# Kernel optimization log

Measured on AMD Instinct MI355X. Metric: run time of the kernel, lower is better.

Reference implementation:

```python
import jax, jax.numpy as jnp
import numpy as np

N, E, C, H, L = 20000, 200000, 64, 4, 2
L0_IN, E_IN, L0_OUT = 65, 15, 64
HC = H * C
EPS = 1e-5  # InstanceNorm1d default eps
NEG_SLOPE = 0.01  # F.leaky_relu default used by DGL EGATConv


def setup_inputs() -> dict:
    key = jax.random.key(0)
    ks = jax.random.split(key, 16)
    def s(k, shape, fan):
        return (jax.random.normal(k, shape, jnp.float32) / np.float32(np.sqrt(fan)))
    return {
        "x": jax.random.normal(ks[0], (N, L0_IN), jnp.float32),
        "efeat": jax.random.normal(ks[1], (E, E_IN), jnp.float32),
        "src": jax.random.randint(ks[2], (E,), 0, N, dtype=jnp.int32),
        "dst": jax.random.randint(ks[3], (E,), 0, N, dtype=jnp.int32),
        "Wn0": s(ks[4], (L0_IN, C), L0_IN),
        "bn0": jnp.zeros((C,), jnp.float32),
        "We0": s(ks[5], (E_IN, C), E_IN),
        "be0": jnp.zeros((C,), jnp.float32),
        "Wnode": s(ks[6], (L, C, HC), C),
        "bnode": jnp.zeros((L, HC), jnp.float32),
        "Wni": s(ks[7], (L, C, HC), C),
        "Wnj": s(ks[8], (L, C, HC), C),
        "Wfij": s(ks[9], (L, C, HC), C),
        "attn": s(ks[10], (L, H, C), C),
        "bias_e": jnp.zeros((L, HC), jnp.float32),
        "Wf": s(ks[11], (C, L0_OUT), C),
        "bf": jnp.zeros((L0_OUT,), jnp.float32),
    }


def _inorm(x):
    # InstanceNorm1d on a 2D [rows, channels] tensor == per-row normalization
    m = jnp.mean(x, axis=-1, keepdims=True)
    v = jnp.var(x, axis=-1, keepdims=True)
    return (x - m) * jax.lax.rsqrt(v + EPS)


def reference(x, efeat, src, dst, Wn0, bn0, We0, be0, Wnode, bnode,
              Wni, Wnj, Wfij, attn, bias_e, Wf, bf):
    h = x @ Wn0 + bn0        # [N, C]
    f = efeat @ We0 + be0    # [E, C]
    for l in range(L):
        # edge feature update: f_out = fc_ni(h)[src] + fc_nj(h)[dst] + fc_fij(f) + bias
        f_out = (h @ Wni[l])[src] + (h @ Wnj[l])[dst] + f @ Wfij[l] + bias_e[l]  # [E, HC]
        e = jax.nn.leaky_relu(f_out, NEG_SLOPE).reshape(E, H, C)
        score = jnp.einsum('ehc,hc->eh', e, attn[l])  # [E, H]
        # edge softmax over incoming edges of each destination node
        smax = jax.ops.segment_max(score, dst, num_segments=N)
        w = jnp.exp(score - smax[dst])
        denom = jax.ops.segment_sum(w, dst, num_segments=N)
        a = w / denom[dst]                                # [E, H]
        hproj = (h @ Wnode[l] + bnode[l]).reshape(N, H, C)
        msg = hproj[src] * a[:, :, None]                  # [E, H, C]
        h_new = jax.ops.segment_sum(msg, dst, num_segments=N)  # [N, H, C]
        # mean over heads -> InstanceNorm -> ELU
        h = jax.nn.elu(_inorm(jnp.mean(h_new, axis=1)))
        f = jax.nn.elu(_inorm(jnp.mean(f_out.reshape(E, H, C), axis=1)))
    return h @ Wf + bf
```

## Files before the change

kernel.cpp:

```cpp
#include <hip/hip_runtime.h>
#include <cmath>

#define NN 20000
#define NE 200000
#define SCAN_BLOCKS 79
#define EBLK 3125
#define EBLK_P 391

typedef __attribute__((ext_vector_type(8))) short bf16x8;
typedef __attribute__((ext_vector_type(4))) float f32x4;
typedef unsigned int uint;

__device__ __forceinline__ float4 ld4(const float* p){ return *(const float4*)p; }

__device__ __forceinline__ uint packbf(float a, float b) {
  uint ua = __float_as_uint(a);
  uint ub = __float_as_uint(b);
  ua = (ua + 0x7fffu + ((ua >> 16) & 1u)) >> 16;
  ub = (ub + 0x7fffu + ((ub >> 16) & 1u)) >> 16;
  return ua | (ub << 16);
}
__device__ __forceinline__ float4 up4(uint2 u) {
  return make_float4(__uint_as_float(u.x << 16), __uint_as_float(u.x & 0xffff0000u),
                     __uint_as_float(u.y << 16), __uint_as_float(u.y & 0xffff0000u));
}

__global__ void gemm16_bf16(const float* __restrict__ A, const float* __restrict__ B,
                            const float* __restrict__ bias, uint2* __restrict__ O,
                            int M, int K, const int* __restrict__ map) {
  int idx = blockIdx.x * 256 + threadIdx.x;
  if (idx >= M * 4) return;
  int m = idx >> 2, jq = idx & 3;
  const float* a = A + (long)m * K;
  const float* b = B + jq * 16;
  float c00=0,c01=0,c02=0,c03=0,c04=0,c05=0,c06=0,c07=0;
  float c08=0,c09=0,c10=0,c11=0,c12=0,c13=0,c14=0,c15=0;
  for (int k = 0; k < K; k++) {
    float av = a[k];
    const float* br = b + (long)k * 64;
    float4 b0 = ld4(br), b1 = ld4(br + 4), b2 = ld4(br + 8), b3 = ld4(br + 12);
    c00 = fmaf(av, b0.x, c00); c01 = fmaf(av, b0.y, c01); c02 = fmaf(av, b0.z, c02); c03 = fmaf(av, b0.w, c03);
    c04 = fmaf(av, b1.x, c04); c05 = fmaf(av, b1.y, c05); c06 = fmaf(av, b1.z, c06); c07 = fmaf(av, b1.w, c07);
    c08 = fmaf(av, b2.x, c08); c09 = fmaf(av, b2.y, c09); c10 = fmaf(av, b2.z, c10); c11 = fmaf(av, b2.w, c11);
    c12 = fmaf(av, b3.x, c12); c13 = fmaf(av, b3.y, c13); c14 = fmaf(av, b3.z, c14); c15 = fmaf(av, b3.w, c15);
  }
  const float* bb = bias + jq * 16;
  float4 v0 = ld4(bb), v1 = ld4(bb + 4), v2 = ld4(bb + 8), v3 = ld4(bb + 12);
  int mo = map ? map[m] : m;
  uint2* op = O + (long)mo * 16 + jq * 4;
  op[0] = make_uint2(packbf(c00 + v0.x, c01 + v0.y), packbf(c02 + v0.z, c03 + v0.w));
  op[1] = make_uint2(packbf(c04 + v1.x, c05 + v1.y), packbf(c06 + v1.z, c07 + v1.w));
  op[2] = make_uint2(packbf(c08 + v2.x, c09 + v2.y), packbf(c10 + v2.z, c11 + v2.w));
  op[3] = make_uint2(packbf(c12 + v3.x, c13 + v3.y), packbf(c14 + v3.z, c15 + v3.w));
}

__global__ void zero_i32(int* __restrict__ p, int n) {
  int i = blockIdx.x * 256 + threadIdx.x;
  if (i < n) p[i] = 0;
}

__global__ void count_deg(const int* __restrict__ dst, int* __restrict__ deg) {
  int e = blockIdx.x * 256 + threadIdx.x;
  if (e < NE) atomicAdd(&deg[dst[e]], 1);
}

__global__ void scan1(const int* __restrict__ deg, int* __restrict__ off, int* __restrict__ bsum) {
  __shared__ int buf[256];
  int t = threadIdx.x;
  int g = blockIdx.x * 256 + t;
  int v = (g < NN) ? deg[g] : 0;
  buf[t] = v;
  __syncthreads();
  for (int s = 1; s < 256; s <<= 1) {
    int x = (t >= s) ? buf[t - s] : 0;
    __syncthreads();
    buf[t] += x;
    __syncthreads();
  }
  if (g < NN) off[g] = buf[t] - v;
  if (t == 255) bsum[blockIdx.x] = buf[255];
}

__global__ void scan2(int* __restrict__ bsum, int* __restrict__ off) {
  __shared__ int buf[128];
  int t = threadIdx.x;
  int v = (t < SCAN_BLOCKS) ? bsum[t] : 0;
  buf[t] = v;
  __syncthreads();
  for (int s = 1; s < 128; s <<= 1) {
    int x = (t >= s) ? buf[t - s] : 0;
    __syncthreads();
    buf[t] += x;
    __syncthreads();
  }
  if (t < SCAN_BLOCKS) bsum[t] = buf[t] - v;
  if (t == 127) off[NN] = buf[127];
}

__global__ void scan3(int* __restrict__ off, const int* __restrict__ bsum) {
  int g = blockIdx.x * 256 + threadIdx.x;
  if (g < NN) off[g] += bsum[blockIdx.x];
}

__global__ void fill_csr(const int* __restrict__ dst, const int* __restrict__ src,
                         const int* __restrict__ off, int* __restrict__ cursor,
                         int* __restrict__ esrc, int* __restrict__ edst,
                         int* __restrict__ csr_pos) {
  int e = blockIdx.x * 256 + threadIdx.x;
  if (e >= NE) return;
  int d = dst[e];
  int p = atomicAdd(&cursor[d], 1);
  int pos = off[d] + p;
  esrc[pos] = src[e];
  edst[pos] = d;
  csr_pos[e] = pos;
}

__global__ void prep_w(const float* __restrict__ Wni, const float* __restrict__ Wnj,
                       const float* __restrict__ Wfij, const float* __restrict__ Wnode,
                       const float* __restrict__ bnode,
                       uint* __restrict__ Wcat, uint* __restrict__ WcT,
                       float* __restrict__ bmean) {
  int rid = blockIdx.x * 256 + threadIdx.x;
  if (rid < 512) {
    int l = rid >> 8, c = rid & 255;
    uint* D = Wcat + (size_t)l * 24576 + c * 96;
    for (int k8 = 0; k8 < 24; k8++) {
      int ss = k8 >> 3;
      const float* S = (ss == 0 ? Wni : ss == 1 ? Wnj : Wfij) + l * 16384;
      int kl = (k8 & 7) * 8;
      uint u0 = packbf(S[(kl+0)*256 + c], S[(kl+1)*256 + c]);
      uint u1 = packbf(S[(kl+2)*256 + c], S[(kl+3)*256 + c]);
      uint u2 = packbf(S[(kl+4)*256 + c], S[(kl+5)*256 + c]);
      uint u3 = packbf(S[(kl+6)*256 + c], S[(kl+7)*256 + c]);
      *((uint4*)(D + k8 * 4)) = make_uint4(u0, u1, u2, u3);
    }
  } else if (rid < 640) {
    int idx = rid - 512;
    int l = idx >> 6, c = idx & 63;
    const float* S = Wnode + l * 16384;
    uint* D = WcT + (size_t)l * 8192 + c * 128;
    for (int kp = 0; kp < 128; kp++) {
      int k0 = kp * 2, k1 = kp * 2 + 1;
      float v0 = S[(k0 & 63) * 256 + (k0 >> 6) * 64 + c] * 0.25f;
      float v1 = S[(k1 & 63) * 256 + (k1 >> 6) * 64 + c] * 0.25f;
      D[kp] = packbf(v0, v1);
    }
  } else if (rid < 768) {
    int idx = rid - 640;
    int l = idx >> 6, c = idx & 63;
    const float* S = bnode + l * 256;
    bmean[l * 64 + c] = 0.25f * (S[c] + S[64 + c] + S[128 + c] + S[192 + c]);
  }
}

__global__ __launch_bounds__(256) void edge_mfma(
    const uint4* __restrict__ f_bf, const uint4* __restrict__ h_bf,
    const uint* __restrict__ Wcat_l, const float* __restrict__ be_l,
    const float* __restrict__ attn_l, const int* __restrict__ esrc,
    const int* __restrict__ edst, float* __restrict__ scc,
    uint4* __restrict__ f_next4)
{
  int nb = (blockIdx.x & 7) * EBLK_P + (blockIdx.x >> 3);
  if (nb >= EBLK) return;
  int base = nb * 64;
  __shared__ uint bstage[2][96 * 36];
  __shared__ float red[4][2][33][6];
  int t = threadIdx.x, lane = t & 63, w = t >> 6;
  int col = lane & 15, quad = lane >> 4;
  int sr = t >> 3, sc = t & 7;
  {
    int e0 = base + sr;
    uint4 vs = h_bf[(long)esrc[e0] * 8 + sc];
    uint4 vd = h_bf[(long)edst[e0] * 8 + sc];
    uint4 vf = f_bf[(long)e0 * 8 + sc];
    *(uint4*)&bstage[0][sr * 36 + sc * 4] = vs;
    *(uint4*)&bstage[0][(32 + sr) * 36 + sc * 4] = vd;
    *(uint4*)&bstage[0][(64 + sr) * 36 + sc * 4] = vf;
  }
  int e1 = base + 32 + sr;
  uint4 v1s = h_bf[(long)esrc[e1] * 8 + sc];
  uint4 v1d = h_bf[(long)edst[e1] * 8 + sc];
  uint4 v1f = f_bf[(long)e1 * 8 + sc];
  __syncthreads();
  float ma[2][2][4];
  #pragma unroll
  for (int ch = 0; ch < 2; ch++) {
    const uint* bp = &bstage[ch][0];
    bf16x8 Ba[6], Bb[6];
    Ba[0] = *(const bf16x8*)&bp[col * 36 + quad * 4];
    Ba[1] = *(const bf16x8*)&bp[col * 36 + 16 + quad * 4];
    Ba[2] = *(const bf16x8*)&bp[(32 + col) * 36 + quad * 4];
    Ba[3] = *(const bf16x8*)&bp[(32 + col) * 36 + 16 + quad * 4];
    Ba[4] = *(const bf16x8*)&bp[(64 + col) * 36 + quad * 4];
    Ba[5] = *(const bf16x8*)&bp[(64 + col) * 36 + 16 + quad * 4];
    Bb[0] = *(const bf16x8*)&bp[(16 + col) * 36 + quad * 4];
    Bb[1] = *(const bf16x8*)&bp[(16 + col) * 36 + 16 + quad * 4];
    Bb[2] = *(const bf16x8*)&bp[(48 + col) * 36 + quad * 4];
    Bb[3] = *(const bf16x8*)&bp[(48 + col) * 36 + 16 + quad * 4];
    Bb[4] = *(const bf16x8*)&bp[(80 + col) * 36 + quad * 4];
    Bb[5] = *(const bf16x8*)&bp[(80 + col) * 36 + 16 + quad * 4];
    float ma0 = 0.f, ma1 = 0.f, ma2 = 0.f, ma3 = 0.f;
    float mb0 = 0.f, mb1 = 0.f, mb2 = 0.f, mb3 = 0.f;
    float sa0 = 0.f, sa1 = 0.f, sa2 = 0.f, sa3 = 0.f;
    float sb0 = 0.f, sb1 = 0.f, sb2 = 0.f, sb3 = 0.f;
    #pragma unroll
    for (int hg = 0; hg < 4; hg++) {
      f32x4 aa = (f32x4){0.f, 0.f, 0.f, 0.f};
      f32x4 ab = (f32x4){0.f, 0.f, 0.f, 0.f};
      const uint* Ab = &Wcat_l[((4 * hg + w) * 16 + col) * 96 + quad * 4];
      #pragma unroll
      for (int kt = 0; kt < 6; kt++) {
        bf16x8 Af = *(const bf16x8*)(Ab + kt * 16);
        aa = __builtin_amdgcn_mfma_f32_16x16x32_bf16(Af, Ba[kt], aa, 0, 0, 0);
        ab = __builtin_amdgcn_mfma_f32_16x16x32_bf16(Af, Bb[kt], ab, 0, 0, 0);
      }
      int ce = (4 * hg + w) * 16 + quad * 4;
      float4 be4 = ld4(be_l + ce);
      float4 at4 = ld4(attn_l + ce);
      float xa0 = aa[0] + be4.x, xa1 = aa[1] + be4.y;
      float xa2 = aa[2] + be4.z, xa3 = aa[3] + be4.w;
      float xb0 = ab[0] + be4.x, xb1 = ab[1] + be4.y;
      float xb2 = ab[2] + be4.z, xb3 = ab[3] + be4.w;
      float la0 = xa0 > 0.f ? xa0 : 0.01f * xa0;
      float la1 = xa1 > 0.f ? xa1 : 0.01f * xa1;
      float la2 = xa2 > 0.f ? xa2 : 0.01f * xa2;
      float la3 = xa3 > 0.f ? xa3 : 0.01f * xa3;
      float lb0 = xb0 > 0.f ? xb0 : 0.01f * xb0;
      float lb1 = xb1 > 0.f ? xb1 : 0.01f * xb1;
      float lb2 = xb2 > 0.f ? xb2 : 0.01f * xb2;
      float lb3 = xb3 > 0.f ? xb3 : 0.01f * xb3;
      float dpa = la0 * at4.x + la1 * at4.y + la2 * at4.z + la3 * at4.w;
      float dpb = lb0 * at4.x + lb1 * at4.y + lb2 * at4.z + lb3 * at4.w;
      if (hg == 0) { sa0 = dpa; sb0 = dpb; }
      else if (hg == 1) { sa1 = dpa; sb1 = dpb; }
      else if (hg == 2) { sa2 = dpa; sb2 = dpb; }
      else { sa3 = dpa; sb3 = dpb; }
      ma0 += xa0; ma1 += xa1; ma2 += xa2; ma3 += xa3;
      mb0 += xb0; mb1 += xb1; mb2 += xb2; mb3 += xb3;
    }
    ma0 *= 0.25f; ma1 *= 0.25f; ma2 *= 0.25f; ma3 *= 0.25f;
    mb0 *= 0.25f; mb1 *= 0.25f; mb2 *= 0.25f; mb3 *= 0.25f;
    ma[ch][0][0] = ma0; ma[ch][0][1] = ma1; ma[ch][0][2] = ma2; ma[ch][0][3] = ma3;
    ma[ch][1][0] = mb0; ma[ch][1][1] = mb1; ma[ch][1][2] = mb2; ma[ch][1][3] = mb3;
    float s1a = ma0 + ma1 + ma2 + ma3;
    float s2a = ma0*ma0 + ma1*ma1 + ma2*ma2 + ma3*ma3;
    float s1b = mb0 + mb1 + mb2 + mb3;
    float s2b = mb0*mb0 + mb1*mb1 + mb2*mb2 + mb3*mb3;
    sa0 += __shfl_xor(sa0, 16); sa0 += __shfl_xor(sa0, 32);
    sa1 += __shfl_xor(sa1, 16); sa1 += __shfl_xor(sa1, 32);
    sa2 += __shfl_xor(sa2, 16); sa2 += __shfl_xor(sa2, 32);
    sa3 += __shfl_xor(sa3, 16); sa3 += __shfl_xor(sa3, 32);
    sb0 += __shfl_xor(sb0, 16); sb0 += __shfl_xor(sb0, 32);
    sb1 += __shfl_xor(sb1, 16); sb1 += __shfl_xor(sb1, 32);
    sb2 += __shfl_xor(sb2, 16); sb2 += __shfl_xor(sb2, 32);
    sb3 += __shfl_xor(sb3, 16); sb3 += __shfl_xor(sb3, 32);
    s1a += __shfl_xor(s1a, 16); s1a += __shfl_xor(s1a, 32);
    s2a += __shfl_xor(s2a, 16); s2a += __shfl_xor(s2a, 32);
    s1b += __shfl_xor(s1b, 16); s1b += __shfl_xor(s1b, 32);
    s2b += __shfl_xor(s2b, 16); s2b += __shfl_xor(s2b, 32);
    if (quad == 0) {
      float* ra = &red[w][ch][col][0];
      ra[0] = sa0; ra[1] = sa1; ra[2] = sa2; ra[3] = sa3; ra[4] = s1a; ra[5] = s2a;
      float* rb = &red[w][ch][16 + col][0];
      rb[0] = sb0; rb[1] = sb1; rb[2] = sb2; rb[3] = sb3; rb[4] = s1b; rb[5] = s2b;
    }
    if (ch == 0) {
      *(uint4*)&bstage[1][sr * 36 + sc * 4] = v1s;
      *(uint4*)&bstage[1][(32 + sr) * 36 + sc * 4] = v1d;
      *(uint4*)&bstage[1][(64 + sr) * 36 + sc * 4] = v1f;
      __syncthreads();
    }
  }
  __syncthreads();
  {
    int eL = t >> 2, hh = t & 3;
    int chx = eL >> 5, c32 = eL & 31;
    float sv = red[0][chx][c32][hh] + red[1][chx][c32][hh]
             + red[2][chx][c32][hh] + red[3][chx][c32][hh];
    scc[(long)(base + eL) * 4 + hh] = sv;
  }
  uint* fout = &bstage[0][0];
  #pragma unroll
  for (int ch = 0; ch < 2; ch++) {
    #pragma unroll
    for (int sub = 0; sub < 2; sub++) {
      int c32 = sub * 16 + col;
      float s1T = red[0][ch][c32][4] + red[1][ch][c32][4]
                + red[2][ch][c32][4] + red[3][ch][c32][4];
      float s2T = red[0][ch][c32][5] + red[1][ch][c32][5]
                + red[2][ch][c32][5] + red[3][ch][c32][5];
      float mean = s1T * 0.015625f;
      float var  = s2T * 0.015625f - mean * mean;
      float rs = rsqrtf(var + 1e-5f);
      float o0 = (ma[ch][sub][0] - mean) * rs; o0 = o0 > 0.f ? o0 : expm1f(o0);
      float o1 = (ma[ch][sub][1] - mean) * rs; o1 = o1 > 0.f ? o1 : expm1f(o1);
      float o2 = (ma[ch][sub][2] - mean) * rs; o2 = o2 > 0.f ? o2 : expm1f(o2);
      float o3 = (ma[ch][sub][3] - mean) * rs; o3 = o3 > 0.f ? o3 : expm1f(o3);
      int eL = ch * 32 + c32;
      fout[eL * 36 + w * 8 + quad * 2]     = packbf(o0, o1);
      fout[eL * 36 + w * 8 + quad * 2 + 1] = packbf(o2, o3);
    }
  }
  __syncthreads();
  {
    int row = t >> 2, part = t & 3;
    uint4 x0 = *(uint4*)&fout[row * 36 + part * 8];
    uint4 x1 = *(uint4*)&fout[row * 36 + part * 8 + 4];
    long gp = ((long)(base + row)) * 8 + part * 2;
    f_next4[gp] = x0;
    f_next4[gp + 1] = x1;
  }
}

__global__ __launch_bounds__(256) void agg_combine(
    const uint2* __restrict__ h2, const float4* __restrict__ sc_csr4,
    const int* __restrict__ esrc, const int* __restrict__ off,
    const uint4* __restrict__ WcT4, const float* __restrict__ bmean_l,
    uint4* __restrict__ h_next4)
{
  __shared__ uint gsh[16][132];
  __shared__ float red2[4][17][2];
  __shared__ uint fout2[16 * 36];
  int t = threadIdx.x, lane = t & 63, w = t >> 6;
  int col = lane & 15, quad = lane >> 4;
  int n0 = blockIdx.x * 16;
  bf16x8 A2[8];
  #pragma unroll
  for (int kt = 0; kt < 8; kt++)
    A2[kt] = *(const bf16x8*)&WcT4[(w * 16 + col) * 32 + kt * 4 + quad];
  #pragma unroll 1
  for (int nl = 0; nl < 4; nl++) {
    int n = n0 + w * 4 + nl;
    int o0 = off[n], o1 = off[n + 1];
    float mx0 = -3.0e38f, mx1 = -3.0e38f, mx2 = -3.0e38f, mx3 = -3.0e38f;
    for (int i = o0 + quad; i < o1; i += 4) {
      float4 s = sc_csr4[i];
      mx0 = fmaxf(mx0, s.x); mx1 = fmaxf(mx1, s.y);
      mx2 = fmaxf(mx2, s.z); mx3 = fmaxf(mx3, s.w);
    }
    mx0 = fmaxf(mx0, __shfl_xor(mx0, 16)); mx0 = fmaxf(mx0, __shfl_xor(mx0, 32));
    mx1 = fmaxf(mx1, __shfl_xor(mx1, 16)); mx1 = fmaxf(mx1, __shfl_xor(mx1, 32));
    mx2 = fmaxf(mx2, __shfl_xor(mx2, 16)); mx2 = fmaxf(mx2, __shfl_xor(mx2, 32));
    mx3 = fmaxf(mx3, __shfl_xor(mx3, 16)); mx3 = fmaxf(mx3, __shfl_xor(mx3, 32));
    float d0 = 0.f, d1 = 0.f, d2 = 0.f, d3 = 0.f;
    float a00=0.f,a01=0.f,a02=0.f,a03=0.f, a10=0.f,a11=0.f,a12=0.f,a13=0.f;
    float a20=0.f,a21=0.f,a22=0.f,a23=0.f, a30=0.f,a31=0.f,a32=0.f,a33=0.f;
    for (int i = o0 + quad; i < o1; i += 4) {
      float4 s = sc_csr4[i];
      float w0 = __expf(s.x - mx0), w1 = __expf(s.y - mx1);
      float w2 = __expf(s.z - mx2), w3 = __expf(s.w - mx3);
      d0 += w0; d1 += w1; d2 += w2; d3 += w3;
      uint2 hv = h2[(long)esrc[i] * 16 + col];
      float4 p = up4(hv);
      a00 = fmaf(w0,p.x,a00); a01 = fmaf(w0,p.y,a01); a02 = fmaf(w0,p.z,a02); a03 = fmaf(w0,p.w,a03);
      a10 = fmaf(w1,p.x,a10); a11 = fmaf(w1,p.y,a11); a12 = fmaf(w1,p.z,a12); a13 = fmaf(w1,p.w,a13);
      a20 = fmaf(w2,p.x,a20); a21 = fmaf(w2,p.y,a21); a22 = fmaf(w2,p.z,a22); a23 = fmaf(w2,p.w,a23);
      a30 = fmaf(w3,p.x,a30); a31 = fmaf(w3,p.y,a31); a32 = fmaf(w3,p.z,a32); a33 = fmaf(w3,p.w,a33);
    }
    d0 += __shfl_xor(d0,16); d0 += __shfl_xor(d0,32);
    d1 += __shfl_xor(d1,16); d1 += __shfl_xor(d1,32);
    d2 += __shfl_xor(d2,16); d2 += __shfl_xor(d2,32);
    d3 += __shfl_xor(d3,16); d3 += __shfl_xor(d3,32);
    a00 += __shfl_xor(a00,16); a00 += __shfl_xor(a00,32);
    a01 += __shfl_xor(a01,16); a01 += __shfl_xor(a01,32);
    a02 += __shfl_xor(a02,16); a02 += __shfl_xor(a02,32);
    a03 += __shfl_xor(a03,16); a03 += __shfl_xor(a03,32);
    a10 += __shfl_xor(a10,16); a10 += __shfl_xor(a10,32);
    a11 += __shfl_xor(a11,16); a11 += __shfl_xor(a11,32);
    a12 += __shfl_xor(a12,16); a12 += __shfl_xor(a12,32);
    a13 += __shfl_xor(a13,16); a13 += __shfl_xor(a13,32);
    a20 += __shfl_xor(a20,16); a20 += __shfl_xor(a20,32);
    a21 += __shfl_xor(a21,16); a21 += __shfl_xor(a21,32);
    a22 += __shfl_xor(a22,16); a22 += __shfl_xor(a22,32);
    a23 += __shfl_xor(a23,16); a23 += __shfl_xor(a23,32);
    a30 += __shfl_xor(a30,16); a30 += __shfl_xor(a30,32);
    a31 += __shfl_xor(a31,16); a31 += __shfl_xor(a31,32);
    a32 += __shfl_xor(a32,16); a32 += __shfl_xor(a32,32);
    a33 += __shfl_xor(a33,16); a33 += __shfl_xor(a33,32);
    uint u0 = 0u, u1 = 0u, u2 = 0u, u3 = 0u, u4 = 0u, u5 = 0u, u6 = 0u, u7 = 0u;
    if (o0 < o1) {
      float i0 = 1.f / d0, i1 = 1.f / d1, i2 = 1.f / d2, i3 = 1.f / d3;
      u0 = packbf(a00*i0, a01*i0); u1 = packbf(a02*i0, a03*i0);
      u2 = packbf(a10*i1, a11*i1); u3 = packbf(a12*i1, a13*i1);
      u4 = packbf(a20*i2, a21*i2); u5 = packbf(a22*i2, a23*i2);
      u6 = packbf(a30*i3, a31*i3); u7 = packbf(a32*i3, a33*i3);
    }
    if (quad == 0) {
      int nloc = w * 4 + nl;
      gsh[nloc][col*2]      = u0; gsh[nloc][col*2 + 1]      = u1;
      gsh[nloc][32 + col*2] = u2; gsh[nloc][32 + col*2 + 1] = u3;
      gsh[nloc][64 + col*2] = u4; gsh[nloc][64 + col*2 + 1] = u5;
      gsh[nloc][96 + col*2] = u6; gsh[nloc][96 + col*2 + 1] = u7;
    }
  }
  __syncthreads();
  f32x4 acc = (f32x4){0.f, 0.f, 0.f, 0.f};
  #pragma unroll
  for (int kt = 0; kt < 8; kt++) {
    bf16x8 Bg = *(const bf16x8*)&gsh[col][kt * 16 + quad * 4];
    acc = __builtin_amdgcn_mfma_f32_16x16x32_bf16(A2[kt], Bg, acc, 0, 0, 0);
  }
  int n2 = n0 + col;
  int dg = off[n2 + 1] - off[n2];
  float4 bm = ld4(bmean_l + w * 16 + quad * 4);
  float x0, x1, x2, x3;
  if (dg > 0) { x0 = acc[0] + bm.x; x1 = acc[1] + bm.y; x2 = acc[2] + bm.z; x3 = acc[3] + bm.w; }
  else { x0 = x1 = x2 = x3 = 0.f; }
  float s1 = x0 + x1 + x2 + x3;
  float s2 = x0*x0 + x1*x1 + x2*x2 + x3*x3;
  s1 += __shfl_xor(s1, 16); s2 += __shfl_xor(s2, 16);
  s1 += __shfl_xor(s1, 32); s2 += __shfl_xor(s2, 32);
  if (quad == 0) { red2[w][col][0] = s1; red2[w][col][1] = s2; }
  __syncthreads();
  float s1T = red2[0][col][0] + red2[1][col][0] + red2[2][col][0] + red2[3][col][0];
  float s2T = red2[0][col][1] + red2[1][col][1] + red2[2][col][1] + red2[3][col][1];
  float mean = s1T * 0.015625f;
  float var  = s2T * 0.015625f - mean * mean;
  float rs = rsqrtf(var + 1e-5f);
  float o0 = (x0 - mean) * rs; o0 = o0 > 0.f ? o0 : expm1f(o0);
  float o1 = (x1 - mean) * rs; o1 = o1 > 0.f ? o1 : expm1f(o1);
  float o2 = (x2 - mean) * rs; o2 = o2 > 0.f ? o2 : expm1f(o2);
  float o3 = (x3 - mean) * rs; o3 = o3 > 0.f ? o3 : expm1f(o3);
  fout2[col * 36 + w * 8 + quad * 2]     = packbf(o0, o1);
  fout2[col * 36 + w * 8 + quad * 2 + 1] = packbf(o2, o3);
  __syncthreads();
  if (t < 128) {
    int row = t >> 3, part = t & 7;
    uint4 x = *(uint4*)&fout2[row * 36 + part * 4];
    h_next4[((long)(n0 + row)) * 8 + part] = x;
  }
}

__global__ void final_gemm(const uint2* __restrict__ h, const float* __restrict__ Wf,
                           const float* __restrict__ bf_, float* __restrict__ out) {
  int idx = blockIdx.x * 256 + threadIdx.x;
  if (idx >= NN * 16) return;
  int m = idx >> 4, j4 = (idx & 15) << 2;
  const uint2* row = h + (long)m * 16;
  float ax = 0.f, ay = 0.f, az = 0.f, aw = 0.f;
  for (int kk = 0; kk < 16; kk++) {
    float4 a = up4(row[kk]);
    float4 b0 = ld4(Wf + (kk * 4 + 0) * 64 + j4);
    float4 b1 = ld4(Wf + (kk * 4 + 1) * 64 + j4);
    float4 b2 = ld4(Wf + (kk * 4 + 2) * 64 + j4);
    float4 b3 = ld4(Wf + (kk * 4 + 3) * 64 + j4);
    ax = fmaf(a.x, b0.x, ax); ay = fmaf(a.x, b0.y, ay); az = fmaf(a.x, b0.z, az); aw = fmaf(a.x, b0.w, aw);
    ax = fmaf(a.y, b1.x, ax); ay = fmaf(a.y, b1.y, ay); az = fmaf(a.y, b1.z, az); aw = fmaf(a.y, b1.w, aw);
    ax = fmaf(a.z, b2.x, ax); ay = fmaf(a.z, b2.y, ay); az = fmaf(a.z, b2.z, az); aw = fmaf(a.z, b2.w, aw);
    ax = fmaf(a.w, b3.x, ax); ay = fmaf(a.w, b3.y, ay); az = fmaf(a.w, b3.z, az); aw = fmaf(a.w, b3.w, aw);
  }
  float4 bb = ld4(bf_ + j4);
  *(float4*)(out + (long)m * 64 + j4) = make_float4(ax + bb.x, ay + bb.y, az + bb.z, aw + bb.w);
}

extern "C" void kernel_launch(void* const* d_in, const int* in_sizes, int n_in,
                              void* d_out, int out_size, void* d_ws, size_t ws_size,
                              hipStream_t stream) {
  const float* x      = (const float*)d_in[0];
  const float* efeat  = (const float*)d_in[1];
  const int*   src    = (const int*)d_in[2];
  const int*   dst    = (const int*)d_in[3];
  const float* Wn0    = (const float*)d_in[4];
  const float* bn0    = (const float*)d_in[5];
  const float* We0    = (const float*)d_in[6];
  const float* be0    = (const float*)d_in[7];
  const float* Wnode  = (const float*)d_in[8];
  const float* bnode  = (const float*)d_in[9];
  const float* Wni    = (const float*)d_in[10];
  const float* Wnj    = (const float*)d_in[11];
  const float* Wfij   = (const float*)d_in[12];
  const float* attn   = (const float*)d_in[13];
  const float* bias_e = (const float*)d_in[14];
  const float* Wf     = (const float*)d_in[15];
  const float* bf     = (const float*)d_in[16];
  float* out = (float*)d_out;

  char* w = (char*)d_ws;
  auto alloc = [&](size_t nbytes) { char* p = w; w += (nbytes + 255) & ~(size_t)255; return p; };
  uint2* h_a   = (uint2*)alloc((size_t)NN * 128);
  uint2* h_b   = (uint2*)alloc((size_t)NN * 128);
  uint2* f_a   = (uint2*)alloc((size_t)NE * 128);
  uint2* f_b   = (uint2*)alloc((size_t)NE * 128);
  float* scc   = (float*)alloc((size_t)NE * 16);
  uint*  Wcat  = (uint*)alloc((size_t)2 * 24576 * 4);
  uint*  WcT   = (uint*)alloc((size_t)2 * 8192 * 4);
  float* bmean = (float*)alloc((size_t)2 * 64 * 4);
  int* deg     = (int*)alloc((size_t)NN * 2 * 4);
  int* cursor  = deg + NN;
  int* off     = (int*)alloc((size_t)(NN + 1) * 4);
  int* esrc    = (int*)alloc((size_t)NE * 4);
  int* edst    = (int*)alloc((size_t)NE * 4);
  int* csr_pos = (int*)alloc((size_t)NE * 4);
  int* bsum    = (int*)alloc((size_t)128 * 4);

  zero_i32<<<(2 * NN + 255) / 256, 256, 0, stream>>>(deg, 2 * NN);
  count_deg<<<(NE + 255) / 256, 256, 0, stream>>>(dst, deg);
  scan1<<<SCAN_BLOCKS, 256, 0, stream>>>(deg, off, bsum);
  scan2<<<1, 128, 0, stream>>>(bsum, off);
  scan3<<<SCAN_BLOCKS, 256, 0, stream>>>(off, bsum);
  fill_csr<<<(NE + 255) / 256, 256, 0, stream>>>(dst, src, off, cursor, esrc, edst, csr_pos);

  gemm16_bf16<<<(NN * 4 + 255) / 256, 256, 0, stream>>>(x, Wn0, bn0, h_a, NN, 65, nullptr);
  gemm16_bf16<<<(NE * 4 + 255) / 256, 256, 0, stream>>>(efeat, We0, be0, f_a, NE, 15, csr_pos);
  prep_w<<<4, 256, 0, stream>>>(Wni, Wnj, Wfij, Wnode, bnode, Wcat, WcT, bmean);

  uint2* hc = h_a; uint2* hn = h_b;
  uint2* fc = f_a; uint2* fn = f_b;
  for (int l = 0; l < 2; l++) {
    const uint* Wcat_l = Wcat + (size_t)l * 24576;
    const uint4* WcT_l = (const uint4*)(WcT + (size_t)l * 8192);
    const float* bm_l  = bmean + (size_t)l * 64;
    const float* be_l  = bias_e + (size_t)l * 256;
    const float* at_l  = attn + (size_t)l * 256;
    edge_mfma<<<8 * EBLK_P, 256, 0, stream>>>((const uint4*)fc, (const uint4*)hc,
                                              Wcat_l, be_l, at_l, esrc, edst, scc,
                                              (uint4*)fn);
    agg_combine<<<NN / 16, 256, 0, stream>>>((const uint2*)hc, (const float4*)scc,
                                             esrc, off, WcT_l, bm_l, (uint4*)hn);
    uint2* tmp = hc; hc = hn; hn = tmp;
    tmp = fc; fc = fn; fn = tmp;
  }
  final_gemm<<<(NN * 16 + 255) / 256, 256, 0, stream>>>(hc, Wf, bf, out);
}
```

Before: 499.5 us.

## Make edge kernel persistent with cross-block prefetch and unroll aggregation loops

Turns edge_mfma into a persistent grid-stride kernel with 768 blocks. Each block prefetches the gathered rows for the next 64-edge block while it computes the current one, so gather latency overlaps with MFMA work and the XCD-aware block remapping is no longer needed. The aggregation loops in agg_combine are unrolled two-wide to expose more memory-level parallelism. The input GEMM's K is made a template parameter and the small GEMM loops get unroll pragmas. The persistent form adds a dedicated fout buffer and an extra barrier per iteration, and it uses fewer blocks than before, which may reduce occupancy.

```diff
diff --git a/kernel.cpp b/kernel.cpp
--- a/kernel.cpp
+++ b/kernel.cpp
@@ -5,7 +5,7 @@
 #define NE 200000
 #define SCAN_BLOCKS 79
 #define EBLK 3125
-#define EBLK_P 391
+#define GRID_E 768
 
 typedef __attribute__((ext_vector_type(8))) short bf16x8;
 typedef __attribute__((ext_vector_type(4))) float f32x4;
@@ -25,9 +25,10 @@
                      __uint_as_float(u.y << 16), __uint_as_float(u.y & 0xffff0000u));
 }
 
+template<int K>
 __global__ void gemm16_bf16(const float* __restrict__ A, const float* __restrict__ B,
                             const float* __restrict__ bias, uint2* __restrict__ O,
-                            int M, int K, const int* __restrict__ map) {
+                            int M, const int* __restrict__ map) {
   int idx = blockIdx.x * 256 + threadIdx.x;
   if (idx >= M * 4) return;
   int m = idx >> 2, jq = idx & 3;
@@ -35,6 +36,7 @@
   const float* b = B + jq * 16;
   float c00=0,c01=0,c02=0,c03=0,c04=0,c05=0,c06=0,c07=0;
   float c08=0,c09=0,c10=0,c11=0,c12=0,c13=0,c14=0,c15=0;
+  #pragma unroll
   for (int k = 0; k < K; k++) {
     float av = a[k];
     const float* br = b + (long)k * 64;
@@ -154,6 +156,92 @@
   }
 }
 
+__device__ __forceinline__ void edge_compute(
+    const uint* bp, const uint* __restrict__ Wcat_l,
+    const float* __restrict__ be_l, const float* __restrict__ attn_l,
+    int w, int col, int quad, int ch,
+    float (&ma)[2][2][4], float (&red)[4][2][33][6])
+{
+  bf16x8 Ba[6], Bb[6];
+  Ba[0] = *(const bf16x8*)&bp[col * 36 + quad * 4];
+  Ba[1] = *(const bf16x8*)&bp[col * 36 + 16 + quad * 4];
+  Ba[2] = *(const bf16x8*)&bp[(32 + col) * 36 + quad * 4];
+  Ba[3] = *(const bf16x8*)&bp[(32 + col) * 36 + 16 + quad * 4];
+  Ba[4] = *(const bf16x8*)&bp[(64 + col) * 36 + quad * 4];
+  Ba[5] = *(const bf16x8*)&bp[(64 + col) * 36 + 16 + quad * 4];
+  Bb[0] = *(const bf16x8*)&bp[(16 + col) * 36 + quad * 4];
+  Bb[1] = *(const bf16x8*)&bp[(16 + col) * 36 + 16 + quad * 4];
+  Bb[2] = *(const bf16x8*)&bp[(48 + col) * 36 + quad * 4];
+  Bb[3] = *(const bf16x8*)&bp[(48 + col) * 36 + 16 + quad * 4];
+  Bb[4] = *(const bf16x8*)&bp[(80 + col) * 36 + quad * 4];
+  Bb[5] = *(const bf16x8*)&bp[(80 + col) * 36 + 16 + quad * 4];
+  float ma0 = 0.f, ma1 = 0.f, ma2 = 0.f, ma3 = 0.f;
+  float mb0 = 0.f, mb1 = 0.f, mb2 = 0.f, mb3 = 0.f;
+  float sa0 = 0.f, sa1 = 0.f, sa2 = 0.f, sa3 = 0.f;
+  float sb0 = 0.f, sb1 = 0.f, sb2 = 0.f, sb3 = 0.f;
+  #pragma unroll
+  for (int hg = 0; hg < 4; hg++) {
+    f32x4 aa = (f32x4){0.f, 0.f, 0.f, 0.f};
+    f32x4 ab = (f32x4){0.f, 0.f, 0.f, 0.f};
+    const uint* Ab = &Wcat_l[((4 * hg + w) * 16 + col) * 96 + quad * 4];
+    #pragma unroll
+    for (int kt = 0; kt < 6; kt++) {
+      bf16x8 Af = *(const bf16x8*)(Ab + kt * 16);
+      aa = __builtin_amdgcn_mfma_f32_16x16x32_bf16(Af, Ba[kt], aa, 0, 0, 0);
+      ab = __builtin_amdgcn_mfma_f32_16x16x32_bf16(Af, Bb[kt], ab, 0, 0, 0);
+    }
+    int ce = (4 * hg + w) * 16 + quad * 4;
+    float4 be4 = ld4(be_l + ce);
+    float4 at4 = ld4(attn_l + ce);
+    float xa0 = aa[0] + be4.x, xa1 = aa[1] + be4.y;
+    float xa2 = aa[2] + be4.z, xa3 = aa[3] + be4.w;
+    float xb0 = ab[0] + be4.x, xb1 = ab[1] + be4.y;
+    float xb2 = ab[2] + be4.z, xb3 = ab[3] + be4.w;
+    float la0 = xa0 > 0.f ? xa0 : 0.01f * xa0;
+    float la1 = xa1 > 0.f ? xa1 : 0.01f * xa1;
+    float la2 = xa2 > 0.f ? xa2 : 0.01f * xa2;
+    float la3 = xa3 > 0.f ? xa3 : 0.01f * xa3;
+    float lb0 = xb0 > 0.f ? xb0 : 0.01f * xb0;
+    float lb1 = xb1 > 0.f ? xb1 : 0.01f * xb1;
+    float lb2 = xb2 > 0.f ? xb2 : 0.01f * xb2;
+    float lb3 = xb3 > 0.f ? xb3 : 0.01f * xb3;
+    float dpa = la0 * at4.x + la1 * at4.y + la2 * at4.z + la3 * at4.w;
+    float dpb = lb0 * at4.x + lb1 * at4.y + lb2 * at4.z + lb3 * at4.w;
+    if (hg == 0) { sa0 = dpa; sb0 = dpb; }
+    else if (hg == 1) { sa1 = dpa; sb1 = dpb; }
+    else if (hg == 2) { sa2 = dpa; sb2 = dpb; }
+    else { sa3 = dpa; sb3 = dpb; }
+    ma0 += xa0; ma1 += xa1; ma2 += xa2; ma3 += xa3;
+    mb0 += xb0; mb1 += xb1; mb2 += xb2; mb3 += xb3;
+  }
+  ma0 *= 0.25f; ma1 *= 0.25f; ma2 *= 0.25f; ma3 *= 0.25f;
+  mb0 *= 0.25f; mb1 *= 0.25f; mb2 *= 0.25f; mb3 *= 0.25f;
+  ma[ch][0][0] = ma0; ma[ch][0][1] = ma1; ma[ch][0][2] = ma2; ma[ch][0][3] = ma3;
+  ma[ch][1][0] = mb0; ma[ch][1][1] = mb1; ma[ch][1][2] = mb2; ma[ch][1][3] = mb3;
+  float s1a = ma0 + ma1 + ma2 + ma3;
+  float s2a = ma0*ma0 + ma1*ma1 + ma2*ma2 + ma3*ma3;
+  float s1b = mb0 + mb1 + mb2 + mb3;
+  float s2b = mb0*mb0 + mb1*mb1 + mb2*mb2 + mb3*mb3;
+  sa0 += __shfl_xor(sa0, 16); sa0 += __shfl_xor(sa0, 32);
+  sa1 += __shfl_xor(sa1, 16); sa1 += __shfl_xor(sa1, 32);
+  sa2 += __shfl_xor(sa2, 16); sa2 += __shfl_xor(sa2, 32);
+  sa3 += __shfl_xor(sa3, 16); sa3 += __shfl_xor(sa3, 32);
+  sb0 += __shfl_xor(sb0, 16); sb0 += __shfl_xor(sb0, 32);
+  sb1 += __shfl_xor(sb1, 16); sb1 += __shfl_xor(sb1, 32);
+  sb2 += __shfl_xor(sb2, 16); sb2 += __shfl_xor(sb2, 32);
+  sb3 += __shfl_xor(sb3, 16); sb3 += __shfl_xor(sb3, 32);
+  s1a += __shfl_xor(s1a, 16); s1a += __shfl_xor(s1a, 32);
+  s2a += __shfl_xor(s2a, 16); s2a += __shfl_xor(s2a, 32);
+  s1b += __shfl_xor(s1b, 16); s1b += __shfl_xor(s1b, 32);
+  s2b += __shfl_xor(s2b, 16); s2b += __shfl_xor(s2b, 32);
+  if (quad == 0) {
+    float* ra = &red[w][ch][col][0];
+    ra[0] = sa0; ra[1] = sa1; ra[2] = sa2; ra[3] = sa3; ra[4] = s1a; ra[5] = s2a;
+    float* rb = &red[w][ch][16 + col][0];
+    rb[0] = sb0; rb[1] = sb1; rb[2] = sb2; rb[3] = sb3; rb[4] = s1b; rb[5] = s2b;
+  }
+}
+
 __global__ __launch_bounds__(256) void edge_mfma(
     const uint4* __restrict__ f_bf, const uint4* __restrict__ h_bf,
     const uint* __restrict__ Wcat_l, const float* __restrict__ be_l,
@@ -161,16 +249,14 @@
     const int* __restrict__ edst, float* __restrict__ scc,
     uint4* __restrict__ f_next4)
 {
-  int nb = (blockIdx.x & 7) * EBLK_P + (blockIdx.x >> 3);
-  if (nb >= EBLK) return;
-  int base = nb * 64;
   __shared__ uint bstage[2][96 * 36];
+  __shared__ uint fout[64 * 36];
   __shared__ float red[4][2][33][6];
   int t = threadIdx.x, lane = t & 63, w = t >> 6;
   int col = lane & 15, quad = lane >> 4;
   int sr = t >> 3, sc = t & 7;
   {
-    int e0 = base + sr;
+    int e0 = blockIdx.x * 64 + sr;
     uint4 vs = h_bf[(long)esrc[e0] * 8 + sc];
     uint4 vd = h_bf[(long)edst[e0] * 8 + sc];
     uint4 vf = f_bf[(long)e0 * 8 + sc];
@@ -178,138 +264,66 @@
     *(uint4*)&bstage[0][(32 + sr) * 36 + sc * 4] = vd;
     *(uint4*)&bstage[0][(64 + sr) * 36 + sc * 4] = vf;
   }
-  int e1 = base + 32 + sr;
-  uint4 v1s = h_bf[(long)esrc[e1] * 8 + sc];
-  uint4 v1d = h_bf[(long)edst[e1] * 8 + sc];
-  uint4 v1f = f_bf[(long)e1 * 8 + sc];
   __syncthreads();
-  float ma[2][2][4];
-  #pragma unroll
-  for (int ch = 0; ch < 2; ch++) {
-    const uint* bp = &bstage[ch][0];
-    bf16x8 Ba[6], Bb[6];
-    Ba[0] = *(const bf16x8*)&bp[col * 36 + quad * 4];
-    Ba[1] = *(const bf16x8*)&bp[col * 36 + 16 + quad * 4];
-    Ba[2] = *(const bf16x8*)&bp[(32 + col) * 36 + quad * 4];
-    Ba[3] = *(const bf16x8*)&bp[(32 + col) * 36 + 16 + quad * 4];
-    Ba[4] = *(const bf16x8*)&bp[(64 + col) * 36 + quad * 4];
-    Ba[5] = *(const bf16x8*)&bp[(64 + col) * 36 + 16 + quad * 4];
-    Bb[0] = *(const bf16x8*)&bp[(16 + col) * 36 + quad * 4];
-    Bb[1] = *(const bf16x8*)&bp[(16 + col) * 36 + 16 + quad * 4];
-    Bb[2] = *(const bf16x8*)&bp[(48 + col) * 36 + quad * 4];
-    Bb[3] = *(const bf16x8*)&bp[(48 + col) * 36 + 16 + quad * 4];
-    Bb[4] = *(const bf16x8*)&bp[(80 + col) * 36 + quad * 4];
-    Bb[5] = *(const bf16x8*)&bp[(80 + col) * 36 + 16 + quad * 4];
-    float ma0 = 0.f, ma1 = 0.f, ma2 = 0.f, ma3 = 0.f;
-    float mb0 = 0.f, mb1 = 0.f, mb2 = 0.f, mb3 = 0.f;
-    float sa0 = 0.f, sa1 = 0.f, sa2 = 0.f, sa3 = 0.f;
-    float sb0 = 0.f, sb1 = 0.f, sb2 = 0.f, sb3 = 0.f;
+  for (int nb = blockIdx.x; nb < EBLK; nb += GRID_E) {
+    int base = nb * 64;
+    int nbn = nb + GRID_E;
+    float ma[2][2][4];
+    int e1 = base + 32 + sr;
+    uint4 p1s = h_bf[(long)esrc[e1] * 8 + sc];
+    uint4 p1d = h_bf[(long)edst[e1] * 8 + sc];
+    uint4 p1f = f_bf[(long)e1 * 8 + sc];
+    edge_compute(&bstage[0][0], Wcat_l, be_l, attn_l, w, col, quad, 0, ma, red);
+    *(uint4*)&bstage[1][sr * 36 + sc * 4] = p1s;
+    *(uint4*)&bstage[1][(32 + sr) * 36 + sc * 4] = p1d;
+    *(uint4*)&bstage[1][(64 + sr) * 36 + sc * 4] = p1f;
+    int e2 = (nbn < EBLK ? nbn : nb) * 64 + sr;
+    uint4 p0s = h_bf[(long)esrc[e2] * 8 + sc];
+    uint4 p0d = h_bf[(long)edst[e2] * 8 + sc];
+    uint4 p0f = f_bf[(long)e2 * 8 + sc];
+    __syncthreads();
+    edge_compute(&bstage[1][0], Wcat_l, be_l, attn_l, w, col, quad, 1, ma, red);
+    __syncthreads();
+    {
+      int eL = t >> 2, hh = t & 3;
+      int chx = eL >> 5, c32 = eL & 31;
+      float sv = red[0][chx][c32][hh] + red[1][chx][c32][hh]
+               + red[2][chx][c32][hh] + red[3][chx][c32][hh];
+      scc[(long)(base + eL) * 4 + hh] = sv;
+    }
     #pragma unroll
-    for (int hg = 0; hg < 4; hg++) {
-      f32x4 aa = (f32x4){0.f, 0.f, 0.f, 0.f};
-      f32x4 ab = (f32x4){0.f, 0.f, 0.f, 0.f};
-      const uint* Ab = &Wcat_l[((4 * hg + w) * 16 + col) * 96 + quad * 4];
+    for (int ch = 0; ch < 2; ch++) {
       #pragma unroll
-      for (int kt = 0; kt < 6; kt++) {
-        bf16x8 Af = *(const bf16x8*)(Ab + kt * 16);
-        aa = __builtin_amdgcn_mfma_f32_16x16x32_bf16(Af, Ba[kt], aa, 0, 0, 0);
-        ab = __builtin_amdgcn_mfma_f32_16x16x32_bf16(Af, Bb[kt], ab, 0, 0, 0);
+      for (int sub = 0; sub < 2; sub++) {
+        int c32 = sub * 16 + col;
+        float s1T = red[0][ch][c32][4] + red[1][ch][c32][4]
+                  + red[2][ch][c32][4] + red[3][ch][c32][4];
+        float s2T = red[0][ch][c32][5] + red[1][ch][c32][5]
+                  + red[2][ch][c32][5] + red[3][ch][c32][5];
+        float mean = s1T * 0.015625f;
+        float var  = s2T * 0.015625f - mean * mean;
+        float rs = rsqrtf(var + 1e-5f);
+        float o0 = (ma[ch][sub][0] - mean) * rs; o0 = o0 > 0.f ? o0 : expm1f(o0);
+        float o1 = (ma[ch][sub][1] - mean) * rs; o1 = o1 > 0.f ? o1 : expm1f(o1);
+        float o2 = (ma[ch][sub][2] - mean) * rs; o2 = o2 > 0.f ? o2 : expm1f(o2);
+        float o3 = (ma[ch][sub][3] - mean) * rs; o3 = o3 > 0.f ? o3 : expm1f(o3);
+        int eL = ch * 32 + c32;
+        fout[eL * 36 + w * 8 + quad * 2]     = packbf(o0, o1);
+        fout[eL * 36 + w * 8 + quad * 2 + 1] = packbf(o2, o3);
       }
-      int ce = (4 * hg + w) * 16 + quad * 4;
-      float4 be4 = ld4(be_l + ce);
-      float4 at4 = ld4(attn_l + ce);
-      float xa0 = aa[0] + be4.x, xa1 = aa[1] + be4.y;
-      float xa2 = aa[2] + be4.z, xa3 = aa[3] + be4.w;
-      float xb0 = ab[0] + be4.x, xb1 = ab[1] + be4.y;
-      float xb2 = ab[2] + be4.z, xb3 = ab[3] + be4.w;
-      float la0 = xa0 > 0.f ? xa0 : 0.01f * xa0;
-      float la1 = xa1 > 0.f ? xa1 : 0.01f * xa1;
-      float la2 = xa2 > 0.f ? xa2 : 0.01f * xa2;
-      float la3 = xa3 > 0.f ? xa3 : 0.01f * xa3;
-      float lb0 = xb0 > 0.f ? xb0 : 0.01f * xb0;
-      float lb1 = xb1 > 0.f ? xb1 : 0.01f * xb1;
-      float lb2 = xb2 > 0.f ? xb2 : 0.01f * xb2;
-      float lb3 = xb3 > 0.f ? xb3 : 0.01f * xb3;
-      float dpa = la0 * at4.x + la1 * at4.y + la2 * at4.z + la3 * at4.w;
-      float dpb = lb0 * at4.x + lb1 * at4.y + lb2 * at4.z + lb3 * at4.w;
-      if (hg == 0) { sa0 = dpa; sb0 = dpb; }
-      else if (hg == 1) { sa1 = dpa; sb1 = dpb; }
-      else if (hg == 2) { sa2 = dpa; sb2 = dpb; }
-      else { sa3 = dpa; sb3 = dpb; }
-      ma0 += xa0; ma1 += xa1; ma2 += xa2; ma3 += xa3;
-      mb0 += xb0; mb1 += xb1; mb2 += xb2; mb3 += xb3;
-    }
-    ma0 *= 0.25f; ma1 *= 0.25f; ma2 *= 0.25f; ma3 *= 0.25f;
-    mb0 *= 0.25f; mb1 *= 0.25f; mb2 *= 0.25f; mb3 *= 0.25f;
-    ma[ch][0][0] = ma0; ma[ch][0][1] = ma1; ma[ch][0][2] = ma2; ma[ch][0][3] = ma3;
-    ma[ch][1][0] = mb0; ma[ch][1][1] = mb1; ma[ch][1][2] = mb2; ma[ch][1][3] = mb3;
-    float s1a = ma0 + ma1 + ma2 + ma3;
-    float s2a = ma0*ma0 + ma1*ma1 + ma2*ma2 + ma3*ma3;
-    float s1b = mb0 + mb1 + mb2 + mb3;
-    float s2b = mb0*mb0 + mb1*mb1 + mb2*mb2 + mb3*mb3;
-    sa0 += __shfl_xor(sa0, 16); sa0 += __shfl_xor(sa0, 32);
-    sa1 += __shfl_xor(sa1, 16); sa1 += __shfl_xor(sa1, 32);
-    sa2 += __shfl_xor(sa2, 16); sa2 += __shfl_xor(sa2, 32);
-    sa3 += __shfl_xor(sa3, 16); sa3 += __shfl_xor(sa3, 32);
-    sb0 += __shfl_xor(sb0, 16); sb0 += __shfl_xor(sb0, 32);
-    sb1 += __shfl_xor(sb1, 16); sb1 += __shfl_xor(sb1, 32);
-    sb2 += __shfl_xor(sb2, 16); sb2 += __shfl_xor(sb2, 32);
-    sb3 += __shfl_xor(sb3, 16); sb3 += __shfl_xor(sb3, 32);
-    s1a += __shfl_xor(s1a, 16); s1a += __shfl_xor(s1a, 32);
-    s2a += __shfl_xor(s2a, 16); s2a += __shfl_xor(s2a, 32);
-    s1b += __shfl_xor(s1b, 16); s1b += __shfl_xor(s1b, 32);
-    s2b += __shfl_xor(s2b, 16); s2b += __shfl_xor(s2b, 32);
-    if (quad == 0) {
-      float* ra = &red[w][ch][col][0];
-      ra[0] = sa0; ra[1] = sa1; ra[2] = sa2; ra[3] = sa3; ra[4] = s1a; ra[5] = s2a;
-      float* rb = &red[w][ch][16 + col][0];
-      rb[0] = sb0; rb[1] = sb1; rb[2] = sb2; rb[3] = sb3; rb[4] = s1b; rb[5] = s2b;
-    }
-    if (ch == 0) {
-      *(uint4*)&bstage[1][sr * 36 + sc * 4] = v1s;
-      *(uint4*)&bstage[1][(32 + sr) * 36 + sc * 4] = v1d;
-      *(uint4*)&bstage[1][(64 + sr) * 36 + sc * 4] = v1f;
-      __syncthreads();
-    }
-  }
-  __syncthreads();
-  {
-    int eL = t >> 2, hh = t & 3;
-    int chx = eL >> 5, c32 = eL & 31;
-    float sv = red[0][chx][c32][hh] + red[1][chx][c32][hh]
-             + red[2][chx][c32][hh] + red[3][chx][c32][hh];
-    scc[(long)(base + eL) * 4 + hh] = sv;
-  }
-  uint* fout = &bstage[0][0];
-  #pragma unroll
-  for (int ch = 0; ch < 2; ch++) {
-    #pragma unroll
-    for (int sub = 0; sub < 2; sub++) {
-      int c32 = sub * 16 + col;
-      float s1T = red[0][ch][c32][4] + red[1][ch][c32][4]
-                + red[2][ch][c32][4] + red[3][ch][c32][4];
-      float s2T = red[0][ch][c32][5] + red[1][ch][c32][5]
-                + red[2][ch][c32][5] + red[3][ch][c32][5];
-      float mean = s1T * 0.015625f;
-      float var  = s2T * 0.015625f - mean * mean;
-      float rs = rsqrtf(var + 1e-5f);
-      float o0 = (ma[ch][sub][0] - mean) * rs; o0 = o0 > 0.f ? o0 : expm1f(o0);
-      float o1 = (ma[ch][sub][1] - mean) * rs; o1 = o1 > 0.f ? o1 : expm1f(o1);
-      float o2 = (ma[ch][sub][2] - mean) * rs; o2 = o2 > 0.f ? o2 : expm1f(o2);
-      float o3 = (ma[ch][sub][3] - mean) * rs; o3 = o3 > 0.f ? o3 : expm1f(o3);
-      int eL = ch * 32 + c32;
-      fout[eL * 36 + w * 8 + quad * 2]     = packbf(o0, o1);
-      fout[eL * 36 + w * 8 + quad * 2 + 1] = packbf(o2, o3);
-    }
-  }
-  __syncthreads();
-  {
-    int row = t >> 2, part = t & 3;
-    uint4 x0 = *(uint4*)&fout[row * 36 + part * 8];
-    uint4 x1 = *(uint4*)&fout[row * 36 + part * 8 + 4];
-    long gp = ((long)(base + row)) * 8 + part * 2;
-    f_next4[gp] = x0;
-    f_next4[gp + 1] = x1;
+    }
+    *(uint4*)&bstage[0][sr * 36 + sc * 4] = p0s;
+    *(uint4*)&bstage[0][(32 + sr) * 36 + sc * 4] = p0d;
+    *(uint4*)&bstage[0][(64 + sr) * 36 + sc * 4] = p0f;
+    __syncthreads();
+    {
+      int row = t >> 2, part = t & 3;
+      uint4 x0 = *(uint4*)&fout[row * 36 + part * 8];
+      uint4 x1 = *(uint4*)&fout[row * 36 + part * 8 + 4];
+      long gp = ((long)(base + row)) * 8 + part * 2;
+      f_next4[gp] = x0;
+      f_next4[gp + 1] = x1;
+    }
   }
 }
 
@@ -334,10 +348,19 @@
     int n = n0 + w * 4 + nl;
     int o0 = off[n], o1 = off[n + 1];
     float mx0 = -3.0e38f, mx1 = -3.0e38f, mx2 = -3.0e38f, mx3 = -3.0e38f;
-    for (int i = o0 + quad; i < o1; i += 4) {
-      float4 s = sc_csr4[i];
-      mx0 = fmaxf(mx0, s.x); mx1 = fmaxf(mx1, s.y);
-      mx2 = fmaxf(mx2, s.z); mx3 = fmaxf(mx3, s.w);
+    {
+      int i = o0 + quad;
+      for (; i + 4 < o1; i += 8) {
+        float4 sA = sc_csr4[i];
+        float4 sB = sc_csr4[i + 4];
+        mx0 = fmaxf(mx0, fmaxf(sA.x, sB.x)); mx1 = fmaxf(mx1, fmaxf(sA.y, sB.y));
+        mx2 = fmaxf(mx2, fmaxf(sA.z, sB.z)); mx3 = fmaxf(mx3, fmaxf(sA.w, sB.w));
+      }
+      if (i < o1) {
+        float4 s = sc_csr4[i];
+        mx0 = fmaxf(mx0, s.x); mx1 = fmaxf(mx1, s.y);
+        mx2 = fmaxf(mx2, s.z); mx3 = fmaxf(mx3, s.w);
+      }
     }
     mx0 = fmaxf(mx0, __shfl_xor(mx0, 16)); mx0 = fmaxf(mx0, __shfl_xor(mx0, 32));
     mx1 = fmaxf(mx1, __shfl_xor(mx1, 16)); mx1 = fmaxf(mx1, __shfl_xor(mx1, 32));
@@ -346,18 +369,24 @@
     float d0 = 0.f, d1 = 0.f, d2 = 0.f, d3 = 0.f;
     float a00=0.f,a01=0.f,a02=0.f,a03=0.f, a10=0.f,a11=0.f,a12=0.f,a13=0.f;
     float a20=0.f,a21=0.f,a22=0.f,a23=0.f, a30=0.f,a31=0.f,a32=0.f,a33=0.f;
-    for (int i = o0 + quad; i < o1; i += 4) {
-      float4 s = sc_csr4[i];
-      float w0 = __expf(s.x - mx0), w1 = __expf(s.y - mx1);
-      float w2 = __expf(s.z - mx2), w3 = __expf(s.w - mx3);
-      d0 += w0; d1 += w1; d2 += w2; d3 += w3;
-      uint2 hv = h2[(long)esrc[i] * 16 + col];
-      float4 p = up4(hv);
-      a00 = fmaf(w0,p.x,a00); a01 = fmaf(w0,p.y,a01); a02 = fmaf(w0,p.z,a02); a03 = fmaf(w0,p.w,a03);
-      a10 = fmaf(w1,p.x,a10); a11 = fmaf(w1,p.y,a11); a12 = fmaf(w1,p.z,a12); a13 = fmaf(w1,p.w,a13);
-      a20 = fmaf(w2,p.x,a20); a21 = fmaf(w2,p.y,a21); a22 = fmaf(w2,p.z,a22); a23 = fmaf(w2,p.w,a23);
-      a30 = fmaf(w3,p.x,a30); a31 = fmaf(w3,p.y,a31); a32 = fmaf(w3,p.z,a32); a33 = fmaf(w3,p.w,a33);
-    }
+    #define AGG_BODY(ii) { \
+      float4 s = sc_csr4[ii]; \
+      int sr_ = esrc[ii]; \
+      uint2 hv = h2[(long)sr_ * 16 + col]; \
+      float w0 = __expf(s.x - mx0), w1 = __expf(s.y - mx1); \
+      float w2 = __expf(s.z - mx2), w3 = __expf(s.w - mx3); \
+      d0 += w0; d1 += w1; d2 += w2; d3 += w3; \
+      float4 p = up4(hv); \
+      a00 = fmaf(w0,p.x,a00); a01 = fmaf(w0,p.y,a01); a02 = fmaf(w0,p.z,a02); a03 = fmaf(w0,p.w,a03); \
+      a10 = fmaf(w1,p.x,a10); a11 = fmaf(w1,p.y,a11); a12 = fmaf(w1,p.z,a12); a13 = fmaf(w1,p.w,a13); \
+      a20 = fmaf(w2,p.x,a20); a21 = fmaf(w2,p.y,a21); a22 = fmaf(w2,p.z,a22); a23 = fmaf(w2,p.w,a23); \
+      a30 = fmaf(w3,p.x,a30); a31 = fmaf(w3,p.y,a31); a32 = fmaf(w3,p.z,a32); a33 = fmaf(w3,p.w,a33); }
+    {
+      int i = o0 + quad;
+      for (; i + 4 < o1; i += 8) { AGG_BODY(i); AGG_BODY(i + 4); }
+      if (i < o1) { AGG_BODY(i); }
+    }
+    #undef AGG_BODY
     d0 += __shfl_xor(d0,16); d0 += __shfl_xor(d0,32);
     d1 += __shfl_xor(d1,16); d1 += __shfl_xor(d1,32);
     d2 += __shfl_xor(d2,16); d2 += __shfl_xor(d2,32);
@@ -439,6 +468,7 @@
   int m = idx >> 4, j4 = (idx & 15) << 2;
   const uint2* row = h + (long)m * 16;
   float ax = 0.f, ay = 0.f, az = 0.f, aw = 0.f;
+  #pragma unroll
   for (int kk = 0; kk < 16; kk++) {
     float4 a = up4(row[kk]);
     float4 b0 = ld4(Wf + (kk * 4 + 0) * 64 + j4);
@@ -501,8 +531,8 @@
   scan3<<<SCAN_BLOCKS, 256, 0, stream>>>(off, bsum);
   fill_csr<<<(NE + 255) / 256, 256, 0, stream>>>(dst, src, off, cursor, esrc, edst, csr_pos);
 
-  gemm16_bf16<<<(NN * 4 + 255) / 256, 256, 0, stream>>>(x, Wn0, bn0, h_a, NN, 65, nullptr);
-  gemm16_bf16<<<(NE * 4 + 255) / 256, 256, 0, stream>>>(efeat, We0, be0, f_a, NE, 15, csr_pos);
+  gemm16_bf16<65><<<(NN * 4 + 255) / 256, 256, 0, stream>>>(x, Wn0, bn0, h_a, NN, nullptr);
+  gemm16_bf16<15><<<(NE * 4 + 255) / 256, 256, 0, stream>>>(efeat, We0, be0, f_a, NE, csr_pos);
   prep_w<<<4, 256, 0, stream>>>(Wni, Wnj, Wfij, Wnode, bnode, Wcat, WcT, bmean);
 
   uint2* hc = h_a; uint2* hn = h_b;
@@ -513,9 +543,9 @@
     const float* bm_l  = bmean + (size_t)l * 64;
     const float* be_l  = bias_e + (size_t)l * 256;
     const float* at_l  = attn + (size_t)l * 256;
-    edge_mfma<<<8 * EBLK_P, 256, 0, stream>>>((const uint4*)fc, (const uint4*)hc,
-                                              Wcat_l, be_l, at_l, esrc, edst, scc,
-                                              (uint4*)fn);
+    edge_mfma<<<GRID_E, 256, 0, stream>>>((const uint4*)fc, (const uint4*)hc,
+                                          Wcat_l, be_l, at_l, esrc, edst, scc,
+                                          (uint4*)fn);
     agg_combine<<<NN / 16, 256, 0, stream>>>((const uint2*)hc, (const float4*)scc,
                                              esrc, off, WcT_l, bm_l, (uint4*)hn);
     uint2* tmp = hc; hc = hn; hn = tmp;
```

Result: slower. 826.5 us (+65.4%).
